# Performance work log

Measured on AMD Instinct MI355X. Metric: run time of the kernel, lower is better.

The kernel has to match this reference:

```python
import jax, jax.numpy as jnp
import numpy as np
import math

B, Q, H, KVH, D, KV, HID = 2, 1024, 32, 8, 128, 4096, 4096

def rotate_half(x):
    x1, x2 = jnp.split(x, 2, axis=-1)
    return jnp.concatenate([-x2, x1], axis=-1)

def setup_inputs() -> dict:
    key = jax.random.key(0)
    ks = jax.random.split(key, 10)
    inv = 1.0 / math.sqrt(HID)
    return {
        "hidden_states": jax.random.normal(ks[0], (B, Q, HID), dtype=jnp.float32),
        "cos": jax.random.uniform(ks[1], (B, 1, Q, D), dtype=jnp.float32),
        "sin": jax.random.uniform(ks[2], (B, 1, Q, D), dtype=jnp.float32),
        "attention_mask": jnp.zeros((B, 1, Q, KV), dtype=jnp.float32),
        "cache_k": jax.random.normal(ks[3], (B, KVH, KV, D), dtype=jnp.float32),
        "cache_v": jax.random.normal(ks[4], (B, KVH, KV, D), dtype=jnp.float32),
        "sink_ids": jnp.arange(Q, dtype=jnp.int32),
        "Wq": jax.random.normal(ks[5], (H * D, HID), dtype=jnp.float32) * inv,
        "Wk": jax.random.normal(ks[6], (KVH * D, HID), dtype=jnp.float32) * inv,
        "Wv": jax.random.normal(ks[7], (KVH * D, HID), dtype=jnp.float32) * inv,
        "Wo": jax.random.normal(ks[8], (HID, H * D), dtype=jnp.float32) * inv,
    }

def reference(hidden_states, cos, sin, attention_mask, cache_k, cache_v, sink_ids, Wq, Wk, Wv, Wo):
    b, q_len, hid = hidden_states.shape
    d = cos.shape[-1]
    h = Wq.shape[0] // d
    kvh = Wk.shape[0] // d
    n_rep = h // kvh

    # projections -> (b, heads, q, d)
    qs = (hidden_states @ Wq.T).reshape(b, q_len, h, d).transpose(0, 2, 1, 3)
    ks = (hidden_states @ Wk.T).reshape(b, q_len, kvh, d).transpose(0, 2, 1, 3)
    vs = (hidden_states @ Wv.T).reshape(b, q_len, kvh, d).transpose(0, 2, 1, 3)

    # RoPE
    qs = qs * cos + rotate_half(qs) * sin
    ks = ks * cos + rotate_half(ks) * sin

    # sink new K/V into the paged cache at sink_ids, then read back the full cache
    k_cache = cache_k.at[:, :, sink_ids, :].set(ks)
    v_cache = cache_v.at[:, :, sink_ids, :].set(vs)

    # repeat_kv: (b, kvh, kv, d) -> (b, h, kv, d)
    k_full = jnp.repeat(k_cache, n_rep, axis=1)
    v_full = jnp.repeat(v_cache, n_rep, axis=1)

    scores = jnp.einsum('bhqd,bhkd->bhqk', qs, k_full) / math.sqrt(d)
    scores = scores + attention_mask
    attn = jax.nn.softmax(scores.astype(jnp.float32), axis=-1).astype(qs.dtype)
    out = jnp.einsum('bhqk,bhkd->bhqd', attn, v_full)
    out = out.transpose(0, 2, 1, 3).reshape(b, q_len, h * d)
    return out @ Wo.T
```

## Files before the change

### kernel.cpp

```cpp
#include <hip/hip_runtime.h>

typedef __bf16 bf16;
typedef __attribute__((ext_vector_type(8))) __bf16 bf16x8;
typedef __attribute__((ext_vector_type(4))) __bf16 bf16x4;
typedef __attribute__((ext_vector_type(4))) float floatx4;

#define LOG2E 1.4426950408889634f

__device__ __forceinline__ void lds16(const void* g, void* l) {
  __builtin_amdgcn_global_load_lds(
      (const __attribute__((address_space(1))) unsigned int*)(unsigned long long)g,
      (__attribute__((address_space(3))) unsigned int*)(unsigned int)(unsigned long long)l,
      16, 0, 0);
}

template <typename CT>
__global__ __launch_bounds__(256) void gemm_bt(const bf16* __restrict__ A,
                                               const bf16* __restrict__ W,
                                               CT* __restrict__ C,
                                               int M, int N, int K) {
  __shared__ bf16 sA[128 * 32];
  __shared__ bf16 sB[128 * 32];
  const int tid = threadIdx.x;
  const int lane = tid & 63;
  const int wave = tid >> 6;
  const int quad = lane >> 4;
  const int l16 = lane & 15;
  const int m0 = blockIdx.y * 128;
  const int n0 = blockIdx.x * 128;
  const int wm = (wave >> 1) * 64;
  const int wn = (wave & 1) * 64;

  floatx4 acc[4][4] = {};

  const int srow = tid >> 2;
  const int cs = tid & 3;
  const int clog = cs ^ ((srow >> 1) & 3);
  const bf16* gA = A + (long)(m0 + srow) * K + clog * 8;
  const bf16* gB = W + (long)(n0 + srow) * K + clog * 8;
  bf16* lA = sA + wave * 512;
  bf16* lB = sB + wave * 512;
  const long step64 = (long)64 * K;
  const int cq = quad ^ ((l16 >> 1) & 3);

  for (int k0 = 0; k0 < K; k0 += 32) {
    lds16(gA, lA);
    lds16(gA + step64, lA + 2048);
    lds16(gB, lB);
    lds16(gB + step64, lB + 2048);
    gA += 32;
    gB += 32;
    __syncthreads();
    bf16x8 af[4], bfr[4];
#pragma unroll
    for (int i = 0; i < 4; ++i)
      af[i] = *(const bf16x8*)(sA + (wm + i * 16 + l16) * 32 + cq * 8);
#pragma unroll
    for (int j = 0; j < 4; ++j)
      bfr[j] = *(const bf16x8*)(sB + (wn + j * 16 + l16) * 32 + cq * 8);
#pragma unroll
    for (int i = 0; i < 4; ++i)
#pragma unroll
      for (int j = 0; j < 4; ++j)
        acc[i][j] = __builtin_amdgcn_mfma_f32_16x16x32_bf16(af[i], bfr[j], acc[i][j], 0, 0, 0);
    __syncthreads();
  }

#pragma unroll
  for (int i = 0; i < 4; ++i) {
    const int row = m0 + wm + i * 16 + quad * 4;
#pragma unroll
    for (int j = 0; j < 4; ++j) {
      const int col = n0 + wn + j * 16 + l16;
#pragma unroll
      for (int r = 0; r < 4; ++r)
        C[(long)(row + r) * N + col] = (CT)acc[i][j][r];
    }
  }
}

__global__ __launch_bounds__(256, 3) void attn(const bf16* __restrict__ qr,
                                               const bf16* __restrict__ kc,
                                               const bf16* __restrict__ vt,
                                               const float* __restrict__ mask,
                                               const int* __restrict__ flag,
                                               bf16* __restrict__ o) {
  __shared__ bf16 sK[64 * 128];
  __shared__ bf16 sV[128 * 64];
  __shared__ bf16 sP[4 * 32 * 64];
  const int tid = threadIdx.x, lane = tid & 63, wave = tid >> 6;
  const int quad = lane >> 4, l16 = lane & 15;

  int id = blockIdx.x;
  const int kvh = id & 7;
  id >>= 3;
  const int b = id & 1;
  id >>= 1;
  const int h = kvh * 4 + (id & 3);
  const int q0 = (id >> 2) * 128;
  const int qw = q0 + wave * 32;

  const bf16* qbase = qr + ((long)(b * 32 + h) * 1024 + qw) * 128;
  bf16x8 qf[2][4];
#pragma unroll
  for (int qt = 0; qt < 2; ++qt)
#pragma unroll
    for (int ks = 0; ks < 4; ++ks)
      qf[qt][ks] = *(const bf16x8*)(qbase + (long)(qt * 16 + l16) * 128 +
                                    ks * 32 + quad * 8);

  floatx4 oacc[8][2] = {};
  float lrun[2] = {0.f, 0.f};

  const float cexp = 0.08838834764831845f * LOG2E;
  const bool use_mask = (*flag != 0);
  const bf16* kbase = kc + (long)(b * 8 + kvh) * 4096 * 128;
  const bf16* vbase = vt + (long)(b * 8 + kvh) * 128 * 4096;
  bf16* sPw = sP + wave * 2048;

  for (int kt = 0; kt < 64; ++kt) {
    const int kv0 = kt * 64;
    __syncthreads();
#pragma unroll
    for (int it = 0; it < 4; ++it) {
      const int r0 = wave * 16 + it * 4;
      const int row = r0 + (lane >> 4);
      lds16(kbase + (long)(kv0 + row) * 128 + (((lane & 15) ^ (row & 15)) << 3),
            sK + r0 * 128);
    }
#pragma unroll
    for (int it = 0; it < 4; ++it) {
      const int r0 = wave * 32 + it * 8;
      const int row = r0 + (lane >> 3);
      lds16(vbase + (long)row * 4096 + kv0 + (((lane & 7) ^ (row & 7)) << 3),
            sV + r0 * 64);
    }
    __syncthreads();

    floatx4 s[4][2] = {};
#pragma unroll
    for (int ks = 0; ks < 4; ++ks)
#pragma unroll
      for (int j = 0; j < 4; ++j) {
        const bf16x8 kf = *(const bf16x8*)(sK + (j * 16 + l16) * 128 +
                                           (((ks * 4 + quad) ^ l16) << 3));
        s[j][0] = __builtin_amdgcn_mfma_f32_16x16x32_bf16(kf, qf[0][ks], s[j][0], 0, 0, 0);
        s[j][1] = __builtin_amdgcn_mfma_f32_16x16x32_bf16(kf, qf[1][ks], s[j][1], 0, 0, 0);
      }

    if (use_mask) {
#pragma unroll
      for (int qt = 0; qt < 2; ++qt)
#pragma unroll
        for (int j = 0; j < 4; ++j)
#pragma unroll
          for (int r = 0; r < 4; ++r) {
            const int q = qw + qt * 16 + l16;
            const int kv = kv0 + j * 16 + quad * 4 + r;
            s[j][qt][r] += mask[((long)b * 1024 + q) * 4096 + kv] * 11.313708498984761f;
          }
    }

#pragma unroll
    for (int qt = 0; qt < 2; ++qt)
#pragma unroll
      for (int j = 0; j < 4; ++j) {
        bf16x4 pk;
#pragma unroll
        for (int r = 0; r < 4; ++r) {
          const float p = exp2f(s[j][qt][r] * cexp);
          lrun[qt] += p;
          pk[r] = (bf16)p;
        }
        *(bf16x4*)(sPw + (qt * 16 + l16) * 64 +
                   (((j * 2 + (quad >> 1)) ^ (l16 & 7)) << 3) + ((quad & 1) << 2)) = pk;
      }

#pragma unroll
    for (int kc2 = 0; kc2 < 2; ++kc2) {
      const int ph = ((kc2 * 4 + quad) ^ (l16 & 7)) << 3;
      const bf16x8 pf0 = *(const bf16x8*)(sPw + l16 * 64 + ph);
      const bf16x8 pf1 = *(const bf16x8*)(sPw + (16 + l16) * 64 + ph);
#pragma unroll
      for (int mt = 0; mt < 8; ++mt) {
        const bf16x8 vf = *(const bf16x8*)(sV + (mt * 16 + l16) * 64 + ph);
        oacc[mt][0] = __builtin_amdgcn_mfma_f32_16x16x32_bf16(vf, pf0, oacc[mt][0], 0, 0, 0);
        oacc[mt][1] = __builtin_amdgcn_mfma_f32_16x16x32_bf16(vf, pf1, oacc[mt][1], 0, 0, 0);
      }
    }
  }

#pragma unroll
  for (int qt = 0; qt < 2; ++qt) {
    float ls = lrun[qt];
    ls += __shfl_xor(ls, 16, 64);
    ls += __shfl_xor(ls, 32, 64);
    const float inv = 1.f / ls;
    const int q = qw + qt * 16 + l16;
    bf16* op = o + ((long)(b * 1024 + q) * 32 + h) * 128 + quad * 4;
#pragma unroll
    for (int mt = 0; mt < 8; ++mt) {
      bf16x4 ov;
#pragma unroll
      for (int r = 0; r < 4; ++r) ov[r] = (bf16)(oacc[mt][qt][r] * inv);
      *(bf16x4*)(op + mt * 16) = ov;
    }
  }
}

__global__ void zeroflag(int* f) { *f = 0; }

__global__ void f2b4(const floatx4* __restrict__ in, bf16x4* __restrict__ out) {
  const long i = (long)blockIdx.x * 256 + threadIdx.x;
  const floatx4 v = in[i];
  bf16x4 o;
  o[0] = (bf16)v[0]; o[1] = (bf16)v[1]; o[2] = (bf16)v[2]; o[3] = (bf16)v[3];
  out[i] = o;
}

__global__ void maskchk(const floatx4* __restrict__ m, int* __restrict__ flag) {
  const long i = (long)blockIdx.x * 256 + threadIdx.x;
  const floatx4 v = m[i];
  if (v[0] != 0.f || v[1] != 0.f || v[2] != 0.f || v[3] != 0.f) atomicOr(flag, 1);
}

__global__ void vtrans(const float* __restrict__ v, bf16* __restrict__ vt) {
  __shared__ float t[32][33];
  const int bk = blockIdx.z;
  const int kv0 = blockIdx.x * 32, d0 = blockIdx.y * 32;
  const int tx = threadIdx.x, ty = threadIdx.y;
  const float* src = v + ((long)bk * 4096 + kv0) * 128 + d0;
#pragma unroll
  for (int k = 0; k < 4; ++k) t[ty * 4 + k][tx] = src[(ty * 4 + k) * 128 + tx];
  __syncthreads();
  bf16* dst = vt + ((long)bk * 128 + d0) * 4096 + kv0;
#pragma unroll
  for (int k = 0; k < 4; ++k) dst[(ty * 4 + k) * 4096 + tx] = (bf16)t[tx][ty * 4 + k];
}

__global__ void rope_q(const bf16* __restrict__ qkv, const float* __restrict__ cosp,
                       const float* __restrict__ sinp, bf16* __restrict__ qrope) {
  const long idx = (long)blockIdx.x * 256 + threadIdx.x;
  const int d = (int)idx & 127;
  const int q = (int)(idx >> 7) & 1023;
  const int h = (int)(idx >> 17) & 31;
  const int b = (int)(idx >> 22);
  const long qrow = ((long)b * 1024 + q) * 6144 + h * 128;
  const float x = (float)qkv[qrow + d];
  const float y = (float)qkv[qrow + (d ^ 64)];
  const long ci = ((long)b * 1024 + q) * 128 + d;
  const float rh = (d < 64) ? -y : y;
  qrope[idx] = (bf16)(x * cosp[ci] + rh * sinp[ci]);
}

__global__ void rope_k(const bf16* __restrict__ qkv, const float* __restrict__ cosp,
                       const float* __restrict__ sinp, const int* __restrict__ sink,
                       bf16* __restrict__ kcb) {
  const long idx = (long)blockIdx.x * 256 + threadIdx.x;
  const int d = (int)idx & 127;
  const int kvh = (int)(idx >> 7) & 7;
  const int q = (int)(idx >> 10) & 1023;
  const int b = (int)(idx >> 20);
  const long krow = ((long)b * 1024 + q) * 6144 + 4096 + kvh * 128;
  const float x = (float)qkv[krow + d];
  const float y = (float)qkv[krow + (d ^ 64)];
  const long ci = ((long)b * 1024 + q) * 128 + d;
  const float rh = (d < 64) ? -y : y;
  const int sk = sink[q];
  kcb[(((long)b * 8 + kvh) * 4096 + sk) * 128 + d] = (bf16)(x * cosp[ci] + rh * sinp[ci]);
}

__global__ void scat_v(const bf16* __restrict__ qkv, const int* __restrict__ sink,
                       bf16* __restrict__ vtb) {
  const long idx = (long)blockIdx.x * 256 + threadIdx.x;
  const int q = (int)idx & 1023;
  const int d = (int)(idx >> 10) & 127;
  const int kvh = (int)(idx >> 17) & 7;
  const int b = (int)(idx >> 20);
  const int sk = sink[q];
  const bf16 val = qkv[((long)b * 1024 + q) * 6144 + 5120 + kvh * 128 + d];
  vtb[(((long)b * 8 + kvh) * 128 + d) * 4096 + sk] = val;
}

extern "C" void kernel_launch(void* const* d_in, const int* in_sizes, int n_in,
                              void* d_out, int out_size, void* d_ws, size_t ws_size,
                              hipStream_t stream) {
  const float* hid  = (const float*)d_in[0];
  const float* cosp = (const float*)d_in[1];
  const float* sinp = (const float*)d_in[2];
  const float* mask = (const float*)d_in[3];
  const float* ck   = (const float*)d_in[4];
  const float* cv   = (const float*)d_in[5];
  const int*   sink = (const int*)d_in[6];
  const float* Wq   = (const float*)d_in[7];
  const float* Wk   = (const float*)d_in[8];
  const float* Wv   = (const float*)d_in[9];
  const float* Wo   = (const float*)d_in[10];
  float* out = (float*)d_out;

  char* ws = (char*)d_ws;
  bf16* wqkv  = (bf16*)(ws);
  bf16* hidb  = (bf16*)(ws + 50331648);
  bf16* qkvb  = (bf16*)(ws + 67108864);
  bf16* qrope = (bf16*)(ws + 92274688);
  bf16* kcb   = (bf16*)(ws + 109051904);
  bf16* vtb   = (bf16*)(ws + 125829120);
  bf16* ob    = (bf16*)(ws + 142606336);
  int*  flag  = (int*)(ws + 159383552);
  bf16* wob   = (bf16*)(ws + 50331648);

  zeroflag<<<1, 1, 0, stream>>>(flag);

  f2b4<<<8192, 256, 0, stream>>>((const floatx4*)hid, (bf16x4*)hidb);
  f2b4<<<16384, 256, 0, stream>>>((const floatx4*)Wq, (bf16x4*)wqkv);
  f2b4<<<4096, 256, 0, stream>>>((const floatx4*)Wk, (bf16x4*)(wqkv + 16777216));
  f2b4<<<4096, 256, 0, stream>>>((const floatx4*)Wv, (bf16x4*)(wqkv + 20971520));
  f2b4<<<8192, 256, 0, stream>>>((const floatx4*)ck, (bf16x4*)kcb);
  maskchk<<<8192, 256, 0, stream>>>((const floatx4*)mask, flag);
  vtrans<<<dim3(128, 4, 16), dim3(32, 8), 0, stream>>>(cv, vtb);

  gemm_bt<bf16><<<dim3(48, 16), 256, 0, stream>>>(hidb, wqkv, qkvb, 2048, 6144, 4096);

  rope_q<<<32768, 256, 0, stream>>>(qkvb, cosp, sinp, qrope);
  rope_k<<<8192, 256, 0, stream>>>(qkvb, cosp, sinp, sink, kcb);
  scat_v<<<8192, 256, 0, stream>>>(qkvb, sink, vtb);

  f2b4<<<16384, 256, 0, stream>>>((const floatx4*)Wo, (bf16x4*)wob);

  attn<<<512, 256, 0, stream>>>(qrope, kcb, vtb, mask, flag, ob);

  gemm_bt<float><<<dim3(32, 16), 256, 0, stream>>>(ob, wob, out, 2048, 4096, 4096);

  (void)in_sizes; (void)n_in; (void)out_size; (void)ws_size;
}
```

Measured before the change: 762.9 us.

## Double-buffer K/V tiles in attention and fold softmax scale into Q RoPE

The attention kernel now keeps two LDS buffers each for K and V. It issues the async global-to-LDS loads for tile kt+1 before computing on tile kt, which replaces the two barriers per iteration with one barrier at the end of the loop. The softmax scale (1/sqrt(d)·log2e) is applied once in rope_q instead of per score, the mask term is rescaled to match, and the row-sum accumulation is vectorised. s_setprio hints are placed around the MFMA sections. The doubled LDS footprint lowers the launch-bounds occupancy target from 3 to 2 blocks per CU, which trades latency hiding between blocks for hiding within a block.

```diff
diff --git a/kernel.cpp b/kernel.cpp
--- a/kernel.cpp
+++ b/kernel.cpp
@@ -6,6 +6,7 @@
 typedef __attribute__((ext_vector_type(4))) float floatx4;
 
 #define LOG2E 1.4426950408889634f
+#define CEXP (0.08838834764831845f * 1.4426950408889634f)
 
 __device__ __forceinline__ void lds16(const void* g, void* l) {
   __builtin_amdgcn_global_load_lds(
@@ -79,14 +80,14 @@
   }
 }
 
-__global__ __launch_bounds__(256, 3) void attn(const bf16* __restrict__ qr,
+__global__ __launch_bounds__(256, 2) void attn(const bf16* __restrict__ qr,
                                                const bf16* __restrict__ kc,
                                                const bf16* __restrict__ vt,
                                                const float* __restrict__ mask,
                                                const int* __restrict__ flag,
                                                bf16* __restrict__ o) {
-  __shared__ bf16 sK[64 * 128];
-  __shared__ bf16 sV[128 * 64];
+  __shared__ bf16 sK[2][64 * 128];
+  __shared__ bf16 sV[2][128 * 64];
   __shared__ bf16 sP[4 * 32 * 64];
   const int tid = threadIdx.x, lane = tid & 63, wave = tid >> 6;
   const int quad = lane >> 4, l16 = lane & 15;
@@ -110,43 +111,51 @@
                                     ks * 32 + quad * 8);
 
   floatx4 oacc[8][2] = {};
-  float lrun[2] = {0.f, 0.f};
-
-  const float cexp = 0.08838834764831845f * LOG2E;
+  floatx4 lrun4[2] = {};
+
   const bool use_mask = (*flag != 0);
   const bf16* kbase = kc + (long)(b * 8 + kvh) * 4096 * 128;
   const bf16* vbase = vt + (long)(b * 8 + kvh) * 128 * 4096;
   bf16* sPw = sP + wave * 2048;
 
-  for (int kt = 0; kt < 64; ++kt) {
+  auto stage = [&](int buf, int kt) {
     const int kv0 = kt * 64;
-    __syncthreads();
 #pragma unroll
     for (int it = 0; it < 4; ++it) {
       const int r0 = wave * 16 + it * 4;
       const int row = r0 + (lane >> 4);
       lds16(kbase + (long)(kv0 + row) * 128 + (((lane & 15) ^ (row & 15)) << 3),
-            sK + r0 * 128);
+            sK[buf] + r0 * 128);
     }
 #pragma unroll
     for (int it = 0; it < 4; ++it) {
       const int r0 = wave * 32 + it * 8;
       const int row = r0 + (lane >> 3);
       lds16(vbase + (long)row * 4096 + kv0 + (((lane & 7) ^ (row & 7)) << 3),
-            sV + r0 * 64);
-    }
-    __syncthreads();
+            sV[buf] + r0 * 64);
+    }
+  };
+
+  stage(0, 0);
+  __syncthreads();
+
+  for (int kt = 0; kt < 64; ++kt) {
+    const int cur = kt & 1;
+    const int kv0 = kt * 64;
+    if (kt < 63) stage(cur ^ 1, kt + 1);
 
     floatx4 s[4][2] = {};
+    __builtin_amdgcn_s_setprio(1);
 #pragma unroll
     for (int ks = 0; ks < 4; ++ks)
 #pragma unroll
       for (int j = 0; j < 4; ++j) {
-        const bf16x8 kf = *(const bf16x8*)(sK + (j * 16 + l16) * 128 +
+        const bf16x8 kf = *(const bf16x8*)(sK[cur] + (j * 16 + l16) * 128 +
                                            (((ks * 4 + quad) ^ l16) << 3));
         s[j][0] = __builtin_amdgcn_mfma_f32_16x16x32_bf16(kf, qf[0][ks], s[j][0], 0, 0, 0);
         s[j][1] = __builtin_amdgcn_mfma_f32_16x16x32_bf16(kf, qf[1][ks], s[j][1], 0, 0, 0);
       }
+    __builtin_amdgcn_s_setprio(0);
 
     if (use_mask) {
 #pragma unroll
@@ -157,7 +166,7 @@
           for (int r = 0; r < 4; ++r) {
             const int q = qw + qt * 16 + l16;
             const int kv = kv0 + j * 16 + quad * 4 + r;
-            s[j][qt][r] += mask[((long)b * 1024 + q) * 4096 + kv] * 11.313708498984761f;
+            s[j][qt][r] += mask[((long)b * 1024 + q) * 4096 + kv] * LOG2E;
           }
     }
 
@@ -166,16 +175,18 @@
 #pragma unroll
       for (int j = 0; j < 4; ++j) {
         bf16x4 pk;
+        floatx4 pv;
 #pragma unroll
         for (int r = 0; r < 4; ++r) {
-          const float p = exp2f(s[j][qt][r] * cexp);
-          lrun[qt] += p;
-          pk[r] = (bf16)p;
+          pv[r] = exp2f(s[j][qt][r]);
+          pk[r] = (bf16)pv[r];
         }
+        lrun4[qt] += pv;
         *(bf16x4*)(sPw + (qt * 16 + l16) * 64 +
                    (((j * 2 + (quad >> 1)) ^ (l16 & 7)) << 3) + ((quad & 1) << 2)) = pk;
       }
 
+    __builtin_amdgcn_s_setprio(1);
 #pragma unroll
     for (int kc2 = 0; kc2 < 2; ++kc2) {
       const int ph = ((kc2 * 4 + quad) ^ (l16 & 7)) << 3;
@@ -183,16 +194,19 @@
       const bf16x8 pf1 = *(const bf16x8*)(sPw + (16 + l16) * 64 + ph);
 #pragma unroll
       for (int mt = 0; mt < 8; ++mt) {
-        const bf16x8 vf = *(const bf16x8*)(sV + (mt * 16 + l16) * 64 + ph);
+        const bf16x8 vf = *(const bf16x8*)(sV[cur] + (mt * 16 + l16) * 64 + ph);
         oacc[mt][0] = __builtin_amdgcn_mfma_f32_16x16x32_bf16(vf, pf0, oacc[mt][0], 0, 0, 0);
         oacc[mt][1] = __builtin_amdgcn_mfma_f32_16x16x32_bf16(vf, pf1, oacc[mt][1], 0, 0, 0);
       }
     }
+    __builtin_amdgcn_s_setprio(0);
+
+    __syncthreads();
   }
 
 #pragma unroll
   for (int qt = 0; qt < 2; ++qt) {
-    float ls = lrun[qt];
+    float ls = (lrun4[qt][0] + lrun4[qt][1]) + (lrun4[qt][2] + lrun4[qt][3]);
     ls += __shfl_xor(ls, 16, 64);
     ls += __shfl_xor(ls, 32, 64);
     const float inv = 1.f / ls;
@@ -250,7 +264,7 @@
   const float y = (float)qkv[qrow + (d ^ 64)];
   const long ci = ((long)b * 1024 + q) * 128 + d;
   const float rh = (d < 64) ? -y : y;
-  qrope[idx] = (bf16)(x * cosp[ci] + rh * sinp[ci]);
+  qrope[idx] = (bf16)((x * cosp[ci] + rh * sinp[ci]) * CEXP);
 }
 
 __global__ void rope_k(const bf16* __restrict__ qkv, const float* __restrict__ cosp,
```

Result: faster. 705.1 us (-7.6%).
